# Optimization experiments

Measured on AMD Instinct MI355X. Metric: run time of the kernel, lower is better.

## Reference

```python
import jax, jax.numpy as jnp
import numpy as np

B, CW_DIM = 256, 8192
DIM_EMBED = 128
DICT_SIZE = 4096
DIM_CODES = CW_DIM // DIM_EMBED  # 64


def setup_inputs() -> dict:
    key = jax.random.key(0)
    k1, k2 = jax.random.split(key)
    x = jax.random.normal(k1, (B, CW_DIM), dtype=jnp.float32)
    dictionary = jax.random.normal(k2, (DIM_CODES, DICT_SIZE, DIM_EMBED), dtype=jnp.float32)
    return {"x": x, "dictionary": dictionary}


def reference(x, dictionary):
    """VQVAE.quantise (eval mode): pairwise sq-distance -> argmin -> gather + one-hot.

    x: [B, cw_dim], dictionary: [C, S, E] with cw_dim = C*E.
    Returns (cw_embed [B, C*E], one_hot_idx [B, C, S]).
    """
    Bb, D = x.shape
    C, S, E = dictionary.shape
    xr = x.reshape(Bb, C, E)                                   # [B, C, E]
    x_sq = jnp.sum(xr * xr, axis=-1, keepdims=True)            # [B, C, 1]
    d_sq = jnp.sum(dictionary * dictionary, axis=-1)           # [C, S]
    cross = jnp.einsum('bce,cse->bcs', xr, dictionary)         # [B, C, S] (GEMM)
    dist = x_sq + d_sq[None, :, :] - 2.0 * cross               # [B, C, S]
    idx = jnp.argmin(dist, axis=-1)                            # [B, C]
    # gather nearest codes: dictionary[c, idx[b,c]] -> [B, C, E]
    code_ids = jnp.arange(C)[None, :]                          # [1, C]
    cw_embed = dictionary[code_ids, idx]                       # [B, C, E]
    cw_embed = cw_embed.reshape(Bb, C * E)                     # [B, cw_dim]
    one_hot_idx = jax.nn.one_hot(idx, S, dtype=x.dtype)        # [B, C, S]
    return cw_embed, one_hot_idx
```

## Files before the change

### kernel.cpp

```cpp
#include <hip/hip_runtime.h>
#include <stdint.h>


#define B_SZ 256
#define C_SZ 64
#define E_SZ 128
#define S_SZ 4096
#define CW   8192
#define TS   128
#define SPB  1024
#define NIT  (SPB / TS)
#define LDB  128

typedef __attribute__((ext_vector_type(4))) float    float4a;
typedef __attribute__((ext_vector_type(8))) _Float16 half8;

__device__ __forceinline__ int swz(int row, int cf16) {
    return row * LDB + (cf16 ^ ((row & 7) << 3));
}

__device__ __forceinline__ void split8(float4a f0, float4a f1, half8& hi, half8& lo) {
    #pragma unroll
    for (int j = 0; j < 4; ++j) {
        _Float16 h0 = (_Float16)f0[j];
        hi[j]     = h0;
        lo[j]     = (_Float16)(f0[j] - (float)h0);
        _Float16 h1 = (_Float16)f1[j];
        hi[4 + j] = h1;
        lo[4 + j] = (_Float16)(f1[j] - (float)h1);
    }
}

__global__ __launch_bounds__(512, 2) void argmin_mfma(
    const float* __restrict__ x,
    const float* __restrict__ dict,
    float* __restrict__ cw_out,
    float* __restrict__ oh)
{
    __shared__ __attribute__((aligned(16))) _Float16 bh[2][TS * LDB];
    __shared__ __attribute__((aligned(16))) _Float16 bl[2][TS * LDB];
    __shared__ __attribute__((aligned(16))) float dsqp[2][TS][4];
    float* rv = reinterpret_cast<float*>(bh);
    int*   ri = reinterpret_cast<int*>(bl);

    const int tid   = threadIdx.x;
    const int lane  = tid & 63;
    const int quad  = lane >> 4;
    const int l15   = lane & 15;
    const int mq    = tid >> 6;
    const int c     = blockIdx.x & 63;
    const int squad = blockIdx.x >> 6;
    const int sbase = squad * SPB;

    int m_attr[4], n_attr[4];
    {
        half8 ones, enc;
        #pragma unroll
        for (int j = 0; j < 8; ++j) { ones[j] = (_Float16)1.0f; enc[j] = (_Float16)(float)l15; }
        float4a z = {0.f, 0.f, 0.f, 0.f};
        float4a pr = __builtin_amdgcn_mfma_f32_16x16x32_f16(enc, ones, z, 0, 0, 0);
        float4a pc = __builtin_amdgcn_mfma_f32_16x16x32_f16(ones, enc, z, 0, 0, 0);
        #pragma unroll
        for (int r = 0; r < 4; ++r) {
            m_attr[r] = (int)(pr[r] * 0.03125f + 0.5f);
            n_attr[r] = (int)(pc[r] * 0.03125f + 0.5f);
        }
    }

    half8 ah[2][4], al[2][4];
    #pragma unroll
    for (int mi = 0; mi < 2; ++mi) {
        int b = mq * 32 + mi * 16 + l15;
        const float* xr = x + (size_t)b * CW + c * E_SZ;
        #pragma unroll
        for (int kk = 0; kk < 4; ++kk) {
            float4a f0 = *reinterpret_cast<const float4a*>(xr + kk * 32 + quad * 8);
            float4a f1 = *reinterpret_cast<const float4a*>(xr + kk * 32 + quad * 8 + 4);
            split8(f0, f1, ah[mi][kk], al[mi][kk]);
        }
    }

    const int srow = tid >> 2;
    const int kq   = (tid & 3) * 32;
    const int q4   = tid & 3;
    const float* drow = dict + ((size_t)c * S_SZ + sbase + srow) * E_SZ + kq;

    float4a pf[8];
    #pragma unroll
    for (int ck = 0; ck < 8; ++ck)
        pf[ck] = *reinterpret_cast<const float4a*>(drow + ck * 4);
    {
        float dp = 0.f;
        #pragma unroll
        for (int ck = 0; ck < 4; ++ck) {
            half8 h, l;
            split8(pf[2 * ck], pf[2 * ck + 1], h, l);
            #pragma unroll
            for (int j = 0; j < 4; ++j) {
                dp = fmaf(pf[2 * ck][j], pf[2 * ck][j], dp);
                dp = fmaf(pf[2 * ck + 1][j], pf[2 * ck + 1][j], dp);
            }
            *reinterpret_cast<half8*>(&bh[0][swz(srow, kq + ck * 8)]) = h;
            *reinterpret_cast<half8*>(&bl[0][swz(srow, kq + ck * 8)]) = l;
        }
        dsqp[0][srow][q4] = dp;
    }

    float bestv[8];
    int   besti[8];
    #pragma unroll
    for (int i = 0; i < 8; ++i) { bestv[i] = 3.4e38f; besti[i] = 0; }

    __syncthreads();

    int cur = 0;
    for (int it = 0; it < NIT; ++it) {
        if (it + 1 < NIT) {
            const float* dr = drow + (size_t)(it + 1) * (TS * E_SZ);
            #pragma unroll
            for (int ck = 0; ck < 8; ++ck)
                pf[ck] = *reinterpret_cast<const float4a*>(dr + ck * 4);
        }

        {
            const int zrow = it * 32 + (tid >> 4);
            const int t4   = tid & 15;
            float* zb = oh + ((size_t)zrow * C_SZ + c) * S_SZ + sbase;
            float4a zz = {0.f, 0.f, 0.f, 0.f};
            #pragma unroll
            for (int j = 0; j < 16; ++j)
                __builtin_nontemporal_store(zz, reinterpret_cast<float4a*>(zb) + t4 + j * 16);
        }

        const _Float16* bhc = bh[cur];
        const _Float16* blc = bl[cur];
        float4a acc[2][8];
        #pragma unroll
        for (int mi = 0; mi < 2; ++mi)
            #pragma unroll
            for (int ni = 0; ni < 8; ++ni)
                acc[mi][ni] = (float4a){0.f, 0.f, 0.f, 0.f};
        __builtin_amdgcn_s_setprio(1);
        #pragma unroll
        for (int kk = 0; kk < 4; ++kk) {
            #pragma unroll
            for (int ni = 0; ni < 8; ++ni) {
                const int sl = ni * 16 + l15;
                half8 bhf = *reinterpret_cast<const half8*>(bhc + swz(sl, kk * 32 + quad * 8));
                half8 blf = *reinterpret_cast<const half8*>(blc + swz(sl, kk * 32 + quad * 8));
                #pragma unroll
                for (int mi = 0; mi < 2; ++mi) {
                    acc[mi][ni] = __builtin_amdgcn_mfma_f32_16x16x32_f16(
                        ah[mi][kk], bhf, acc[mi][ni], 0, 0, 0);
                    acc[mi][ni] = __builtin_amdgcn_mfma_f32_16x16x32_f16(
                        ah[mi][kk], blf, acc[mi][ni], 0, 0, 0);
                    acc[mi][ni] = __builtin_amdgcn_mfma_f32_16x16x32_f16(
                        al[mi][kk], bhf, acc[mi][ni], 0, 0, 0);
                }
            }
        }
        __builtin_amdgcn_s_setprio(0);

        #pragma unroll
        for (int ni = 0; ni < 8; ++ni)
            #pragma unroll
            for (int r = 0; r < 4; ++r) {
                const int sl = ni * 16 + n_attr[r];
                float4a qa = *reinterpret_cast<const float4a*>(&dsqp[cur][sl][0]);
                float dsq = (qa[0] + qa[1]) + (qa[2] + qa[3]);
                int sg = sbase + it * TS + sl;
                #pragma unroll
                for (int mi = 0; mi < 2; ++mi) {
                    float dist = dsq - 2.0f * acc[mi][ni][r];
                    int slot = mi * 4 + r;
                    if (dist < bestv[slot]) { bestv[slot] = dist; besti[slot] = sg; }
                }
            }

        if (it + 1 < NIT) {
            const int nb = cur ^ 1;
            float dp = 0.f;
            #pragma unroll
            for (int ck = 0; ck < 4; ++ck) {
                half8 h, l;
                split8(pf[2 * ck], pf[2 * ck + 1], h, l);
                #pragma unroll
                for (int j = 0; j < 4; ++j) {
                    dp = fmaf(pf[2 * ck][j], pf[2 * ck][j], dp);
                    dp = fmaf(pf[2 * ck + 1][j], pf[2 * ck + 1][j], dp);
                }
                *reinterpret_cast<half8*>(&bh[nb][swz(srow, kq + ck * 8)]) = h;
                *reinterpret_cast<half8*>(&bl[nb][swz(srow, kq + ck * 8)]) = l;
            }
            dsqp[nb][srow][q4] = dp;
        }
        __syncthreads();
        cur ^= 1;
    }


    #pragma unroll
    for (int mi = 0; mi < 2; ++mi)
        #pragma unroll
        for (int r = 0; r < 4; ++r) {
            int row = mq * 32 + mi * 16 + m_attr[r];
            int col = n_attr[r];
            rv[col * 256 + row] = bestv[mi * 4 + r];
            ri[col * 256 + row] = besti[mi * 4 + r];
        }
    __syncthreads();

    if (tid < 256) {
        float bv = 3.4e38f; int bi = 0x7fffffff;
        #pragma unroll 4
        for (int j = 0; j < 16; ++j) {
            float v = rv[j * 256 + tid];
            int   i = ri[j * 256 + tid];
            if (v < bv || (v == bv && i < bi)) { bv = v; bi = i; }
        }
        float* cp = cw_out + (size_t)tid * CW + c * E_SZ + squad * 2;
        cp[0] = bv;
        cp[1] = __int_as_float(bi);
    }
}

__global__ __launch_bounds__(256) void finalize(
    const float* __restrict__ dict,
    float* __restrict__ cw_out,
    float* __restrict__ oh)
{
    __shared__ int fid[64];
    const int c     = blockIdx.x & 63;
    const int btile = blockIdx.x >> 6;
    const int tid   = threadIdx.x;

    if (tid < 64) {
        const int row = btile * 64 + tid;
        const float* cp = cw_out + (size_t)row * CW + c * E_SZ;
        float bv = cp[0]; int bi = __float_as_int(cp[1]);
        #pragma unroll
        for (int k = 1; k < 4; ++k) {
            float v = cp[2 * k];
            if (v < bv) { bv = v; bi = __float_as_int(cp[2 * k + 1]); }
        }
        fid[tid] = bi;
        oh[((size_t)row * C_SZ + c) * S_SZ + bi] = 1.0f;
    }
    __syncthreads();

    const int row = tid >> 2, q = tid & 3;
    const int bi = fid[row];
    const float4a* src = reinterpret_cast<const float4a*>(
        dict + ((size_t)c * S_SZ + bi) * E_SZ) + q * 8;
    float4a* dst = reinterpret_cast<float4a*>(
        cw_out + (size_t)(btile * 64 + row) * CW + c * E_SZ) + q * 8;
    #pragma unroll
    for (int j = 0; j < 8; ++j) dst[j] = src[j];
}

extern "C" void kernel_launch(void* const* d_in, const int* in_sizes, int n_in,
                              void* d_out, int out_size, void* d_ws, size_t ws_size,
                              hipStream_t stream) {
    const float* x    = (const float*)d_in[0];
    const float* dict = (const float*)d_in[1];
    float* out = (float*)d_out;
    float* oh  = out + (size_t)B_SZ * CW;

    argmin_mfma<<<dim3(256), dim3(512), 0, stream>>>(x, dict, out, oh);
    finalize<<<dim3(256), dim3(256), 0, stream>>>(dict, out, oh);
}
```

Measured before the change: 485.7 us.

## Replace LDS-staged dictionary tiles with per-wave register streaming and shuffle reductions

New measurement: 568.5 us. 17.1% more time.

```diff
diff --git a/kernel.cpp b/kernel.cpp
--- a/kernel.cpp
+++ b/kernel.cpp
@@ -7,17 +7,11 @@
 #define E_SZ 128
 #define S_SZ 4096
 #define CW   8192
-#define TS   128
 #define SPB  1024
-#define NIT  (SPB / TS)
-#define LDB  128
+#define NCH  (SPB / 16)
 
 typedef __attribute__((ext_vector_type(4))) float    float4a;
 typedef __attribute__((ext_vector_type(8))) _Float16 half8;
-
-__device__ __forceinline__ int swz(int row, int cf16) {
-    return row * LDB + (cf16 ^ ((row & 7) << 3));
-}
 
 __device__ __forceinline__ void split8(float4a f0, float4a f1, half8& hi, half8& lo) {
     #pragma unroll
@@ -31,28 +25,24 @@
     }
 }
 
-__global__ __launch_bounds__(512, 2) void argmin_mfma(
+__global__ __launch_bounds__(256, 4) void argmin_mfma(
     const float* __restrict__ x,
     const float* __restrict__ dict,
     float* __restrict__ cw_out,
     float* __restrict__ oh)
 {
-    __shared__ __attribute__((aligned(16))) _Float16 bh[2][TS * LDB];
-    __shared__ __attribute__((aligned(16))) _Float16 bl[2][TS * LDB];
-    __shared__ __attribute__((aligned(16))) float dsqp[2][TS][4];
-    float* rv = reinterpret_cast<float*>(bh);
-    int*   ri = reinterpret_cast<int*>(bl);
-
     const int tid   = threadIdx.x;
     const int lane  = tid & 63;
     const int quad  = lane >> 4;
     const int l15   = lane & 15;
-    const int mq    = tid >> 6;
+    const int w     = tid >> 6;
     const int c     = blockIdx.x & 63;
-    const int squad = blockIdx.x >> 6;
+    const int btile = (blockIdx.x >> 6) & 3;
+    const int squad = blockIdx.x >> 8;
     const int sbase = squad * SPB;
-
-    int m_attr[4], n_attr[4];
+    const int rowbase = btile * 64 + w * 16;
+
+    int mpack = 0, npack = 0;
     {
         half8 ones, enc;
         #pragma unroll
@@ -62,165 +52,122 @@
         float4a pc = __builtin_amdgcn_mfma_f32_16x16x32_f16(ones, enc, z, 0, 0, 0);
         #pragma unroll
         for (int r = 0; r < 4; ++r) {
-            m_attr[r] = (int)(pr[r] * 0.03125f + 0.5f);
-            n_attr[r] = (int)(pc[r] * 0.03125f + 0.5f);
-        }
-    }
-
-    half8 ah[2][4], al[2][4];
-    #pragma unroll
-    for (int mi = 0; mi < 2; ++mi) {
-        int b = mq * 32 + mi * 16 + l15;
-        const float* xr = x + (size_t)b * CW + c * E_SZ;
+            mpack |= ((int)(pr[r] * 0.03125f + 0.5f)) << (8 * r);
+            npack |= ((int)(pc[r] * 0.03125f + 0.5f)) << (8 * r);
+        }
+    }
+
+    half8 ah[4], al[4];
+    {
+        const float* xr = x + (size_t)(rowbase + l15) * CW + c * E_SZ;
         #pragma unroll
         for (int kk = 0; kk < 4; ++kk) {
             float4a f0 = *reinterpret_cast<const float4a*>(xr + kk * 32 + quad * 8);
             float4a f1 = *reinterpret_cast<const float4a*>(xr + kk * 32 + quad * 8 + 4);
-            split8(f0, f1, ah[mi][kk], al[mi][kk]);
-        }
-    }
-
-    const int srow = tid >> 2;
-    const int kq   = (tid & 3) * 32;
-    const int q4   = tid & 3;
-    const float* drow = dict + ((size_t)c * S_SZ + sbase + srow) * E_SZ + kq;
+            split8(f0, f1, ah[kk], al[kk]);
+        }
+    }
+
+    const float* dl = dict + ((size_t)c * S_SZ + sbase + l15) * E_SZ + quad * 8;
+
+    float bestv[4];
+    int   besti[4];
+    #pragma unroll
+    for (int r = 0; r < 4; ++r) { bestv[r] = 3.4e38f; besti[r] = 0; }
 
     float4a pf[8];
     #pragma unroll
-    for (int ck = 0; ck < 8; ++ck)
-        pf[ck] = *reinterpret_cast<const float4a*>(drow + ck * 4);
+    for (int kk = 0; kk < 4; ++kk) {
+        pf[2 * kk]     = *reinterpret_cast<const float4a*>(dl + kk * 32);
+        pf[2 * kk + 1] = *reinterpret_cast<const float4a*>(dl + kk * 32 + 4);
+    }
+    half8 bhf[4], blf[4];
+    float dqf;
     {
         float dp = 0.f;
         #pragma unroll
-        for (int ck = 0; ck < 4; ++ck) {
-            half8 h, l;
-            split8(pf[2 * ck], pf[2 * ck + 1], h, l);
+        for (int kk = 0; kk < 4; ++kk) {
+            split8(pf[2 * kk], pf[2 * kk + 1], bhf[kk], blf[kk]);
             #pragma unroll
             for (int j = 0; j < 4; ++j) {
-                dp = fmaf(pf[2 * ck][j], pf[2 * ck][j], dp);
-                dp = fmaf(pf[2 * ck + 1][j], pf[2 * ck + 1][j], dp);
-            }
-            *reinterpret_cast<half8*>(&bh[0][swz(srow, kq + ck * 8)]) = h;
-            *reinterpret_cast<half8*>(&bl[0][swz(srow, kq + ck * 8)]) = l;
-        }
-        dsqp[0][srow][q4] = dp;
-    }
-
-    float bestv[8];
-    int   besti[8];
-    #pragma unroll
-    for (int i = 0; i < 8; ++i) { bestv[i] = 3.4e38f; besti[i] = 0; }
-
-    __syncthreads();
-
-    int cur = 0;
-    for (int it = 0; it < NIT; ++it) {
-        if (it + 1 < NIT) {
-            const float* dr = drow + (size_t)(it + 1) * (TS * E_SZ);
+                dp = fmaf(pf[2 * kk][j], pf[2 * kk][j], dp);
+                dp = fmaf(pf[2 * kk + 1][j], pf[2 * kk + 1][j], dp);
+            }
+        }
+        float t = dp + __shfl_xor(dp, 16, 64);
+        dqf = t + __shfl_xor(t, 32, 64);
+    }
+
+    for (int ch = 0; ch < NCH; ++ch) {
+        if (ch + 1 < NCH) {
+            const float* dn = dl + (size_t)(ch + 1) * 16 * E_SZ;
             #pragma unroll
-            for (int ck = 0; ck < 8; ++ck)
-                pf[ck] = *reinterpret_cast<const float4a*>(dr + ck * 4);
+            for (int kk = 0; kk < 4; ++kk) {
+                pf[2 * kk]     = *reinterpret_cast<const float4a*>(dn + kk * 32);
+                pf[2 * kk + 1] = *reinterpret_cast<const float4a*>(dn + kk * 32 + 4);
+            }
         }
 
         {
-            const int zrow = it * 32 + (tid >> 4);
-            const int t4   = tid & 15;
-            float* zb = oh + ((size_t)zrow * C_SZ + c) * S_SZ + sbase;
+            const int zrow = rowbase + (ch >> 2);
+            float* zb = oh + ((size_t)zrow * C_SZ + c) * S_SZ + sbase + (ch & 3) * 256;
             float4a zz = {0.f, 0.f, 0.f, 0.f};
-            #pragma unroll
-            for (int j = 0; j < 16; ++j)
-                __builtin_nontemporal_store(zz, reinterpret_cast<float4a*>(zb) + t4 + j * 16);
-        }
-
-        const _Float16* bhc = bh[cur];
-        const _Float16* blc = bl[cur];
-        float4a acc[2][8];
-        #pragma unroll
-        for (int mi = 0; mi < 2; ++mi)
-            #pragma unroll
-            for (int ni = 0; ni < 8; ++ni)
-                acc[mi][ni] = (float4a){0.f, 0.f, 0.f, 0.f};
-        __builtin_amdgcn_s_setprio(1);
+            __builtin_nontemporal_store(zz, reinterpret_cast<float4a*>(zb) + lane);
+        }
+
+        float4a acc = {0.f, 0.f, 0.f, 0.f};
         #pragma unroll
         for (int kk = 0; kk < 4; ++kk) {
-            #pragma unroll
-            for (int ni = 0; ni < 8; ++ni) {
-                const int sl = ni * 16 + l15;
-                half8 bhf = *reinterpret_cast<const half8*>(bhc + swz(sl, kk * 32 + quad * 8));
-                half8 blf = *reinterpret_cast<const half8*>(blc + swz(sl, kk * 32 + quad * 8));
-                #pragma unroll
-                for (int mi = 0; mi < 2; ++mi) {
-                    acc[mi][ni] = __builtin_amdgcn_mfma_f32_16x16x32_f16(
-                        ah[mi][kk], bhf, acc[mi][ni], 0, 0, 0);
-                    acc[mi][ni] = __builtin_amdgcn_mfma_f32_16x16x32_f16(
-                        ah[mi][kk], blf, acc[mi][ni], 0, 0, 0);
-                    acc[mi][ni] = __builtin_amdgcn_mfma_f32_16x16x32_f16(
-                        al[mi][kk], bhf, acc[mi][ni], 0, 0, 0);
-                }
-            }
-        }
-        __builtin_amdgcn_s_setprio(0);
-
-        #pragma unroll
-        for (int ni = 0; ni < 8; ++ni)
-            #pragma unroll
-            for (int r = 0; r < 4; ++r) {
-                const int sl = ni * 16 + n_attr[r];
-                float4a qa = *reinterpret_cast<const float4a*>(&dsqp[cur][sl][0]);
-                float dsq = (qa[0] + qa[1]) + (qa[2] + qa[3]);
-                int sg = sbase + it * TS + sl;
-                #pragma unroll
-                for (int mi = 0; mi < 2; ++mi) {
-                    float dist = dsq - 2.0f * acc[mi][ni][r];
-                    int slot = mi * 4 + r;
-                    if (dist < bestv[slot]) { bestv[slot] = dist; besti[slot] = sg; }
-                }
-            }
-
-        if (it + 1 < NIT) {
-            const int nb = cur ^ 1;
+            acc = __builtin_amdgcn_mfma_f32_16x16x32_f16(ah[kk], bhf[kk], acc, 0, 0, 0);
+            acc = __builtin_amdgcn_mfma_f32_16x16x32_f16(ah[kk], blf[kk], acc, 0, 0, 0);
+            acc = __builtin_amdgcn_mfma_f32_16x16x32_f16(al[kk], bhf[kk], acc, 0, 0, 0);
+        }
+
+        #pragma unroll
+        for (int r = 0; r < 4; ++r) {
+            const int na = (npack >> (8 * r)) & 15;
+            float dsq = __shfl(dqf, (lane & 48) | na, 64);
+            int sg = sbase + ch * 16 + na;
+            float dist = dsq - 2.0f * acc[r];
+            if (dist < bestv[r]) { bestv[r] = dist; besti[r] = sg; }
+        }
+
+        if (ch + 1 < NCH) {
             float dp = 0.f;
             #pragma unroll
-            for (int ck = 0; ck < 4; ++ck) {
-                half8 h, l;
-                split8(pf[2 * ck], pf[2 * ck + 1], h, l);
+            for (int kk = 0; kk < 4; ++kk) {
+                split8(pf[2 * kk], pf[2 * kk + 1], bhf[kk], blf[kk]);
                 #pragma unroll
                 for (int j = 0; j < 4; ++j) {
-                    dp = fmaf(pf[2 * ck][j], pf[2 * ck][j], dp);
-                    dp = fmaf(pf[2 * ck + 1][j], pf[2 * ck + 1][j], dp);
+                    dp = fmaf(pf[2 * kk][j], pf[2 * kk][j], dp);
+                    dp = fmaf(pf[2 * kk + 1][j], pf[2 * kk + 1][j], dp);
                 }
-                *reinterpret_cast<half8*>(&bh[nb][swz(srow, kq + ck * 8)]) = h;
-                *reinterpret_cast<half8*>(&bl[nb][swz(srow, kq + ck * 8)]) = l;
-            }
-            dsqp[nb][srow][q4] = dp;
-        }
-        __syncthreads();
-        cur ^= 1;
-    }
-
-
-    #pragma unroll
-    for (int mi = 0; mi < 2; ++mi)
-        #pragma unroll
-        for (int r = 0; r < 4; ++r) {
-            int row = mq * 32 + mi * 16 + m_attr[r];
-            int col = n_attr[r];
-            rv[col * 256 + row] = bestv[mi * 4 + r];
-            ri[col * 256 + row] = besti[mi * 4 + r];
-        }
-    __syncthreads();
-
-    if (tid < 256) {
-        float bv = 3.4e38f; int bi = 0x7fffffff;
-        #pragma unroll 4
-        for (int j = 0; j < 16; ++j) {
-            float v = rv[j * 256 + tid];
-            int   i = ri[j * 256 + tid];
-            if (v < bv || (v == bv && i < bi)) { bv = v; bi = i; }
-        }
-        float* cp = cw_out + (size_t)tid * CW + c * E_SZ + squad * 2;
-        cp[0] = bv;
-        cp[1] = __int_as_float(bi);
+            }
+            float t = dp + __shfl_xor(dp, 16, 64);
+            dqf = t + __shfl_xor(t, 32, 64);
+        }
+    }
+
+    #pragma unroll
+    for (int m = 1; m < 16; m <<= 1) {
+        #pragma unroll
+        for (int r = 0; r < 4; ++r) {
+            float ov = __shfl_xor(bestv[r], m, 64);
+            int   oi = __shfl_xor(besti[r], m, 64);
+            if (ov < bestv[r] || (ov == bestv[r] && oi < besti[r])) {
+                bestv[r] = ov; besti[r] = oi;
+            }
+        }
+    }
+
+    if (l15 == 0) {
+        #pragma unroll
+        for (int r = 0; r < 4; ++r) {
+            const int row = rowbase + ((mpack >> (8 * r)) & 15);
+            float* cp = cw_out + (size_t)row * CW + c * E_SZ + squad * 2;
+            cp[0] = bestv[r];
+            cp[1] = __int_as_float(besti[r]);
+        }
     }
 }
 
@@ -266,6 +213,6 @@
     float* out = (float*)d_out;
     float* oh  = out + (size_t)B_SZ * CW;
 
-    argmin_mfma<<<dim3(256), dim3(512), 0, stream>>>(x, dict, out, oh);
+    argmin_mfma<<<dim3(1024), dim3(256), 0, stream>>>(x, dict, out, oh);
     finalize<<<dim3(256), dim3(256), 0, stream>>>(dict, out, oh);
 }
```
